# Optimization experiments

Hardware: AMD Instinct MI355X
Metric: run time of the kernel (lower is better)

The kernel has to match this reference:

```python
import jax, jax.numpy as jnp
import numpy as np

# Model hyperparams (match init_kwargs)
D_MODEL = 1024
D_STATE = 128
D_CONV = 4
EXPAND = 2
HEADDIM = 64
NGROUPS = 1
D_INNER = EXPAND * D_MODEL          # 2048
D_SSM = D_INNER                     # d_ssm=None -> d_inner; d_mlp = 0
NHEADS = D_SSM // HEADDIM           # 32
CONV_DIM = D_SSM + 2 * NGROUPS * D_STATE            # 2304
D_IN_PROJ = 2 * D_INNER + 2 * NGROUPS * D_STATE + NHEADS  # 4384
GROUP_SIZE = D_SSM // NGROUPS
EPS = 1e-5
HEAD_TO_GROUP = np.arange(NHEADS) // (NHEADS // NGROUPS)


def silu(x):
    return x * jax.nn.sigmoid(x)


def setup_inputs() -> dict:
    key = jax.random.key(0)
    ks = jax.random.split(key, 10)
    B, L = 16, 512
    u = jax.random.normal(ks[0], (B, L, D_MODEL), jnp.float32)
    # in_proj (bias=False): weight [d_in_proj, d_model]
    W_in = jax.random.normal(ks[1], (D_IN_PROJ, D_MODEL), jnp.float32) / np.sqrt(D_MODEL)
    # depthwise causal conv1d: weight [conv_dim, 1, d_conv], bias [conv_dim]
    conv_w = jax.random.normal(ks[2], (CONV_DIM, 1, D_CONV), jnp.float32) / np.sqrt(D_CONV)
    conv_b = jax.random.normal(ks[3], (CONV_DIM,), jnp.float32) * 0.01
    # recurrent feedback weights (zero-init in torch; small random here to exercise the path)
    W_rxbc = jax.random.normal(ks[4], (CONV_DIM, D_SSM), jnp.float32) * (0.01 / np.sqrt(D_SSM))
    W_rdt = jax.random.normal(ks[5], (NHEADS, D_SSM), jnp.float32) * (0.01 / np.sqrt(D_SSM))
    # dt_bias = inverse-softplus of dt ~ U_log[1e-3, 1e-1]
    dt = jnp.exp(jax.random.uniform(ks[6], (NHEADS,)) * (np.log(0.1) - np.log(0.001)) + np.log(0.001))
    dt_bias = dt + jnp.log(-jnp.expm1(-dt))
    A_log = jnp.log(jax.random.uniform(ks[7], (NHEADS,), minval=1.0, maxval=16.0))
    D_param = jnp.ones((NHEADS,), jnp.float32)
    norm_w = jnp.ones((D_SSM,), jnp.float32)
    W_out = jax.random.normal(ks[8], (D_MODEL, D_INNER), jnp.float32) / np.sqrt(D_INNER)
    return dict(u=u, W_in=W_in, conv_w=conv_w, conv_b=conv_b, W_rxbc=W_rxbc,
                W_rdt=W_rdt, dt_bias=dt_bias, A_log=A_log, D_param=D_param,
                norm_w=norm_w, W_out=W_out)


def _forward(u, W_in, conv_w, conv_b, W_rxbc, W_rdt, dt_bias, A_log, D_param, norm_w, W_out):
    B, L, _ = u.shape
    zxbcdt = jnp.einsum('bld,ed->ble', u, W_in)  # [B,L,d_in_proj]; d_mlp=0 so no z0/x0
    z, xBC_u, dt_raw = jnp.split(zxbcdt, [D_SSM, D_SSM + CONV_DIM], axis=-1)
    # causal depthwise conv over time (torch Conv1d pad=d_conv-1, truncated to L)
    xp = jnp.pad(xBC_u, ((0, 0), (D_CONV - 1, 0), (0, 0)))
    xBC_conv = conv_b + sum(xp[:, k:k + L, :] * conv_w[:, 0, k] for k in range(D_CONV))
    A = -jnp.exp(A_log.astype(jnp.float32))  # [H]

    def step(carry, inp):
        state, y_prev = carry            # state: [B,H,P,N] f32, y_prev: [B,d_ssm]
        xBC_t, dt_t, z_t = inp
        xBC = silu(xBC_t + y_prev @ W_rxbc.T)        # recurrent xBC feedback
        dtr = silu(dt_t + y_prev @ W_rdt.T)          # recurrent dt feedback
        x_t = xBC[:, :D_SSM]
        Bv = xBC[:, D_SSM:D_SSM + NGROUPS * D_STATE]
        Cv = xBC[:, D_SSM + NGROUPS * D_STATE:]
        dt = jax.nn.softplus(dtr + dt_bias).astype(jnp.float32)  # [B,H]; dt_limit=(0,inf) -> no clamp
        dA = jnp.exp(dt * A)                                     # [B,H]
        x_h = x_t.reshape(B, NHEADS, HEADDIM).astype(jnp.float32)
        B_hn = Bv.reshape(B, NGROUPS, D_STATE).astype(jnp.float32)[:, HEAD_TO_GROUP, :]
        C_hn = Cv.reshape(B, NGROUPS, D_STATE).astype(jnp.float32)[:, HEAD_TO_GROUP, :]
        state = state * dA[:, :, None, None] + dt[:, :, None, None] * x_h[:, :, :, None] * B_hn[:, :, None, :]
        y = (state * C_hn[:, :, None, :]).sum(-1) + D_param[None, :, None] * x_h  # [B,H,P]
        y = y.reshape(B, D_SSM)
        # gated RMSNorm (norm_before_gate=False): rmsnorm(y*silu(z)) * weight, groupwise
        g = y * silu(z_t)
        gg = g.reshape(B, NGROUPS, GROUP_SIZE)
        ms = jnp.mean(gg * gg, axis=-1, keepdims=True)
        yn = (gg * jax.lax.rsqrt(ms + EPS)).reshape(B, D_SSM) * norm_w
        out_t = yn @ W_out.T
        return (state, yn), out_t

    state0 = jnp.zeros((B, NHEADS, HEADDIM, D_STATE), jnp.float32)
    y0 = jnp.zeros((B, D_SSM), u.dtype)
    xs = (jnp.swapaxes(xBC_conv, 0, 1), jnp.swapaxes(dt_raw, 0, 1), jnp.swapaxes(z, 0, 1))
    _, out = jax.lax.scan(step, (state0, y0), xs)  # out: [L,B,d_model]
    return jnp.swapaxes(out, 0, 1)


def reference(u, W_in, conv_w, conv_b, W_rxbc, W_rdt, dt_bias, A_log, D_param, norm_w, W_out):
    return _forward(u, W_in, conv_w, conv_b, W_rxbc, W_rdt, dt_bias, A_log, D_param, norm_w, W_out)
```

## Files before the change

### kernel.cpp

```cpp
#include <hip/hip_runtime.h>

typedef __attribute__((ext_vector_type(8))) short short8;
typedef __attribute__((ext_vector_type(4))) float floatx4;

#define BQ 16
#define LQ 512
#define DM 1024
#define DPROJ 4384
#define RAWC 2336
#define KD 2048
#define NWG 128
#define NTHR 512
#define AWG 73

#define AFLAG_BASE 16384
#define BAR_U32 35072

__device__ __forceinline__ float siluf(float x) { return x / (1.f + __expf(-x)); }
__device__ __forceinline__ float softplusf(float x) { return (x > 20.f) ? x : log1pf(__expf(x)); }
__device__ __forceinline__ unsigned short f2bf(float f) {
    union { float f; unsigned u; } v; v.f = f;
    unsigned r = v.u + 0x7FFFu + ((v.u >> 16) & 1u);
    return (unsigned short)(r >> 16);
}

__global__ void cvt_bf16_kernel(const float* __restrict__ s, unsigned short* __restrict__ d, int n) {
    int i = blockIdx.x * 256 + threadIdx.x;
    if (i < n) d[i] = f2bf(s[i]);
}

__global__ void pack_weights_kernel(const float* __restrict__ rxbc, const float* __restrict__ rdt,
                                    const float* __restrict__ wout, unsigned short* __restrict__ wall) {
    long i = (long)blockIdx.x * 256 + threadIdx.x;
    if (i >= 3360L * KD) return;
    int c = (int)(i >> 11), k = (int)(i & 2047);
    const float* src = (c < 2304) ? rxbc + (long)c * KD + k
                     : (c < 2336) ? rdt + (long)(c - 2304) * KD + k
                     :              wout + (long)(c - 2336) * KD + k;
    wall[i] = f2bf(*src);
}

__global__ __launch_bounds__(256) void gemm_inproj_kernel(const short* __restrict__ A,
                                                          const short* __restrict__ Bw,
                                                          float* __restrict__ C) {
    const int lane = threadIdx.x & 63, wave = threadIdx.x >> 6;
    const int row = lane & 15, q = lane >> 4;
    const long m0 = (long)blockIdx.x * 128 + wave * 16;
    const long n0 = (long)blockIdx.y * 32;
    const short* ap0 = A + (m0 + row) * DM + q * 8;
    const short* ap1 = ap0 + 64 * DM;
    const short* bp0 = Bw + (n0 + row) * DM + q * 8;
    const short* bp1 = bp0 + 16 * DM;
    floatx4 acc00 = {0.f,0.f,0.f,0.f}, acc01 = {0.f,0.f,0.f,0.f};
    floatx4 acc10 = {0.f,0.f,0.f,0.f}, acc11 = {0.f,0.f,0.f,0.f};
    for (int k = 0; k < DM; k += 32) {
        short8 a0 = *(const short8*)(ap0 + k);
        short8 a1 = *(const short8*)(ap1 + k);
        short8 b0 = *(const short8*)(bp0 + k);
        short8 b1 = *(const short8*)(bp1 + k);
        acc00 = __builtin_amdgcn_mfma_f32_16x16x32_bf16(a0, b0, acc00, 0, 0, 0);
        acc01 = __builtin_amdgcn_mfma_f32_16x16x32_bf16(a0, b1, acc01, 0, 0, 0);
        acc10 = __builtin_amdgcn_mfma_f32_16x16x32_bf16(a1, b0, acc10, 0, 0, 0);
        acc11 = __builtin_amdgcn_mfma_f32_16x16x32_bf16(a1, b1, acc11, 0, 0, 0);
    }
    float* cp0 = C + (m0 + q * 4) * DPROJ + n0 + row;
    float* cp1 = cp0 + 64 * DPROJ;
    #pragma unroll
    for (int r = 0; r < 4; ++r) {
        cp0[(long)r * DPROJ]      = acc00[r];
        cp0[(long)r * DPROJ + 16] = acc01[r];
        cp1[(long)r * DPROJ]      = acc10[r];
        cp1[(long)r * DPROJ + 16] = acc11[r];
    }
}

__global__ void setup_zero_kernel(unsigned* ghist, float* msum, unsigned* bar) {
    int i = blockIdx.x * 256 + threadIdx.x;
    if (i < 16384) ghist[i] = 0u;
    if (i < 4096) msum[i] = 0.f;
    if (i < BAR_U32) bar[i] = 0u;
}

__global__ __launch_bounds__(NTHR, 1) void scan_kernel(
    const float* __restrict__ zx,
    float* __restrict__ raw,
    unsigned short* __restrict__ ghist,
    float* __restrict__ msum,
    unsigned* __restrict__ bar,
    const short* __restrict__ wall,
    float* __restrict__ scale_hist,
    const float* __restrict__ dt_bias, const float* __restrict__ A_log,
    const float* __restrict__ D_param, const float* __restrict__ norm_w,
    const float* __restrict__ conv_w, const float* __restrict__ conv_b,
    float* __restrict__ out)
{
    const int w = blockIdx.x, tid = threadIdx.x;
    const int lane = tid & 63, wv = tid >> 6;

    __shared__ float redu[2][8][16][16];
    __shared__ float bc_lds[2][128];
    __shared__ float ypart[4][64];

    const bool doA = (w < AWG);
    const int colr = lane & 15, q = lane >> 4;
    const unsigned long long* gq = (const unsigned long long*)ghist;
    const int abase = colr * 512 + wv * 64 + q * 2;
    const int r_tl = tid >> 8, r_idx = tid & 255, r_orow = r_idx >> 4, r_col = r_idx & 15;
    const unsigned* aspin = bar + ((((lane >> 2) * 8 + wv) * 4) + (lane & 3)) * 32;

    short8 wr0[8], wr1[8];
    if (doA) {
        const short* wp0 = wall + ((long)((2 * w    ) * 16 + colr) * KD + wv * 256 + q * 8);
        const short* wp1 = wall + ((long)((2 * w + 1) * 16 + colr) * KD + wv * 256 + q * 8);
        #pragma unroll
        for (int ks = 0; ks < 8; ++ks) {
            wr0[ks] = *(const short8*)(wp0 + ks * 32);
            wr1[ks] = *(const short8*)(wp1 + ks * 32);
        }
    }

    const int b = w >> 3;
    const int j = w & 7;
    const int h = j * 4 + (wv >> 1);
    const int half = wv & 1;
    float s[64];
    #pragma unroll
    for (int i = 0; i < 64; ++i) s[i] = 0.f;
    const float Aneg = -__expf(A_log[h]);
    const float dtb  = dt_bias[h];
    const float Dp   = D_param[h];
    const float nw   = norm_w[h * 64 + lane];
    const int cx = h * 64 + lane;
    const float4 cwx = *(const float4*)(conv_w + cx * 4);
    const float cbx = conv_b[cx];
    const int bcw = tid >> 7, bcn = tid & 127;
    const int cbc = 2048 + bcw * 128 + bcn;
    float4 cwbc = {0.f,0.f,0.f,0.f}; float cbbc = 0.f;
    if (tid < 256) { cwbc = *(const float4*)(conv_w + cbc * 4); cbbc = conv_b[cbc]; }
    float xh1 = 0.f, xh2 = 0.f, xh3 = 0.f, bh1 = 0.f, bh2 = 0.f, bh3 = 0.f;

    int sp_off = -1; unsigned sp_base = 0;
    {
        const int bq4 = b >> 2;
        if      (lane == 0) { sp_off = AFLAG_BASE + ((2*h  )*8 +     bq4) * 32; sp_base = 1; }
        else if (lane == 1) { sp_off = AFLAG_BASE + ((2*h+1)*8 +     bq4) * 32; sp_base = 1; }
        else if (lane == 2) { sp_off = AFLAG_BASE + ((2*h  )*8 + 4 + bq4) * 32; sp_base = 1; }
        else if (lane == 3) { sp_off = AFLAG_BASE + ((2*h+1)*8 + 4 + bq4) * 32; sp_base = 1; }
        else if (lane == 4) { sp_off = AFLAG_BASE + (72*8 + (h >= 16 ? 4 : 0) + bq4) * 32; sp_base = 1; }
        else if (wv < 4 && lane == 5) { sp_off = AFLAG_BASE + ((64+2*wv)*8 +     bq4) * 32; sp_base = 1; }
        else if (wv < 4 && lane == 6) { sp_off = AFLAG_BASE + ((65+2*wv)*8 +     bq4) * 32; sp_base = 1; }
        else if (wv < 4 && lane == 7) { sp_off = AFLAG_BASE + ((64+2*wv)*8 + 4 + bq4) * 32; sp_base = 1; }
        else if (wv < 4 && lane == 8) { sp_off = AFLAG_BASE + ((65+2*wv)*8 + 4 + bq4) * 32; sp_base = 1; }
        else if (lane >= 9 && lane < 41) {
            sp_off = ((b * 8 + ((lane - 9) >> 2)) * 4 + ((lane - 9) & 3)) * 32; sp_base = 0;
        }
    }
    const unsigned* bspin = bar + (sp_off < 0 ? 0 : sp_off);

    for (int t = 0; t < LQ; ++t) {
        const long zr = ((long)b * LQ + t) * DPROJ;
        float xq  = zx[zr + 2048 + cx];
        float zq  = zx[zr + cx];
        float dzq = zx[zr + 4352 + h];
        float bq = 0.f;
        if (tid < 256) bq = zx[zr + 2048 + cbc];

        if (doA) {
            while (__hip_atomic_load(aspin, __ATOMIC_RELAXED, __HIP_MEMORY_SCOPE_AGENT)
                   < (unsigned)t) {}
            unsigned long long ar[16];
            const long gb0 = (long)t * 8192 + abase;
            #pragma unroll
            for (int ks = 0; ks < 8; ++ks) {
                ar[2 * ks]     = __hip_atomic_load(gq + gb0 + ks * 8,
                                 __ATOMIC_RELAXED, __HIP_MEMORY_SCOPE_AGENT);
                ar[2 * ks + 1] = __hip_atomic_load(gq + gb0 + ks * 8 + 1,
                                 __ATOMIC_RELAXED, __HIP_MEMORY_SCOPE_AGENT);
            }
            floatx4 acc0 = {0.f,0.f,0.f,0.f}, acc1 = {0.f,0.f,0.f,0.f};
            #pragma unroll
            for (int ks = 0; ks < 8; ++ks) {
                union { unsigned long long u[2]; short8 s8; } af;
                af.u[0] = ar[2 * ks]; af.u[1] = ar[2 * ks + 1];
                acc0 = __builtin_amdgcn_mfma_f32_16x16x32_bf16(af.s8, wr0[ks], acc0, 0, 0, 0);
                acc1 = __builtin_amdgcn_mfma_f32_16x16x32_bf16(af.s8, wr1[ks], acc1, 0, 0, 0);
            }
            #pragma unroll
            for (int r = 0; r < 4; ++r) {
                redu[0][wv][q * 4 + r][colr] = acc0[r];
                redu[1][wv][q * 4 + r][colr] = acc1[r];
            }
            __syncthreads();
            float v = 0.f;
            #pragma unroll
            for (int kq = 0; kq < 8; ++kq) v += redu[r_tl][kq][r_orow][r_col];
            int gc = (2 * w + r_tl) * 16 + r_col;
            __hip_atomic_store(raw + (t & 1) * (16 * RAWC) + r_orow * RAWC + gc, v,
                               __ATOMIC_RELAXED, __HIP_MEMORY_SCOPE_AGENT);
            asm volatile("s_waitcnt vmcnt(0)" ::: "memory");
            if (lane == 0)
                __hip_atomic_store(bar + AFLAG_BASE + (w * 8 + wv) * 32, (unsigned)(t + 1),
                                   __ATOMIC_RELAXED, __HIP_MEMORY_SCOPE_AGENT);
            __syncthreads();
        }

        if (sp_off >= 0) {
            while (__hip_atomic_load(bspin, __ATOMIC_RELAXED, __HIP_MEMORY_SCOPE_AGENT)
                   < sp_base + (unsigned)t) {}
        }
        const float* rawb = raw + (t & 1) * (16 * RAWC) + b * RAWC;
        float bcval = 0.f;
        if (tid < 256) bcval = __hip_atomic_load(rawb + 2048 + bcw * 128 + bcn,
                                                 __ATOMIC_RELAXED, __HIP_MEMORY_SCOPE_AGENT);
        float xr   = __hip_atomic_load(rawb + cx,       __ATOMIC_RELAXED, __HIP_MEMORY_SCOPE_AGENT);
        float dtrr = __hip_atomic_load(rawb + 2304 + h, __ATOMIC_RELAXED, __HIP_MEMORY_SCOPE_AGENT);
        const float* mp = msum + ((t + 7) & 7) * 512 + b * 32;
        float msv = 0.f;
        #pragma unroll
        for (int k = 0; k < 32; ++k)
            msv += __hip_atomic_load(mp + k, __ATOMIC_RELAXED, __HIP_MEMORY_SCOPE_AGENT);
        float rs = rsqrtf(msv * (1.f / 2048.f) + 1e-5f);
        if (j == 0 && tid == 0 && t >= 1)
            __hip_atomic_store(scale_hist + b * LQ + (t - 1), rs,
                               __ATOMIC_RELAXED, __HIP_MEMORY_SCOPE_AGENT);
        if (tid < 256) {
            float pre = cbbc + bh3 * cwbc.x + bh2 * cwbc.y + bh1 * cwbc.z + bq * cwbc.w;
            bc_lds[bcw][bcn] = siluf(pre + rs * bcval);
            bh3 = bh2; bh2 = bh1; bh1 = bq;
        }
        float xpre = cbx + xh3 * cwx.x + xh2 * cwx.y + xh1 * cwx.z + xq * cwx.w;
        xh3 = xh2; xh2 = xh1; xh1 = xq;
        float xv = siluf(xpre + rs * xr);
        float dt = softplusf(siluf(dzq + rs * dtrr) + dtb);
        float dA = __expf(dt * Aneg);
        float zg = siluf(zq);
        __syncthreads();

        float dtx = dt * xv, yac = 0.f;
        const floatx4* Bp = (const floatx4*)&bc_lds[0][half * 64];
        const floatx4* Cp = (const floatx4*)&bc_lds[1][half * 64];
        #pragma unroll
        for (int i = 0; i < 16; ++i) {
            floatx4 b4 = Bp[i], c4 = Cp[i];
            s[4*i+0] = s[4*i+0] * dA + dtx * b4.x; yac += s[4*i+0] * c4.x;
            s[4*i+1] = s[4*i+1] * dA + dtx * b4.y; yac += s[4*i+1] * c4.y;
            s[4*i+2] = s[4*i+2] * dA + dtx * b4.z; yac += s[4*i+2] * c4.z;
            s[4*i+3] = s[4*i+3] * dA + dtx * b4.w; yac += s[4*i+3] * c4.w;
        }
        if (half) ypart[wv >> 1][lane] = yac;
        __syncthreads();
        if (!half) {
            float y = yac + ypart[wv >> 1][lane] + Dp * xv;
            float g = y * zg;
            unsigned gb = (unsigned)f2bf(g * nw);
            unsigned up = __shfl_down(gb, 1);
            if (!(lane & 1))
                __hip_atomic_store((unsigned*)ghist + ((long)(t + 1) * 16384
                                   + ((b * KD + h * 64 + lane) >> 1)),
                                   gb | (up << 16), __ATOMIC_RELAXED, __HIP_MEMORY_SCOPE_AGENT);
            float sq = g * g;
            #pragma unroll
            for (int off = 32; off; off >>= 1) sq += __shfl_xor(sq, off, 64);
            if (lane == 0)
                __hip_atomic_store(msum + ((t & 7) * 512 + b * 32 + j * 4 + (wv >> 1)), sq,
                                   __ATOMIC_RELAXED, __HIP_MEMORY_SCOPE_AGENT);
            asm volatile("s_waitcnt vmcnt(0)" ::: "memory");
            if (lane == 0)
                __hip_atomic_store(bar + (w * 4 + (wv >> 1)) * 32, (unsigned)(t + 1),
                                   __ATOMIC_RELAXED, __HIP_MEMORY_SCOPE_AGENT);
        }
    }

    {
        const unsigned* fp = bar + tid * 32;
        while (__hip_atomic_load(fp, __ATOMIC_RELAXED, __HIP_MEMORY_SCOPE_AGENT) < 512u) {}
    }
    __syncthreads();
    {
        const int vb = w * 2 + (tid >> 8);
        const int vt = tid & 255;
        const int vwv = vt >> 6, vlane = vt & 63;
        const int vcolr = vlane & 15, vq = vlane >> 4;
        for (int it = 0; it < 8; ++it) {
            const int idx = vb * 8 + it;
            const int tt = idx >> 2;
            const int n0 = (idx & 3) * 256 + vwv * 64;
            const long ab = (long)(tt + 1) * 8192 + vcolr * 512 + vq * 2;
            const short* bp = wall + ((long)(2336 + n0 + vcolr) * KD + vq * 8);
            const unsigned long long* gq2 = (const unsigned long long*)ghist;
            floatx4 acc0 = {0.f,0.f,0.f,0.f}, acc1 = {0.f,0.f,0.f,0.f};
            floatx4 acc2 = {0.f,0.f,0.f,0.f}, acc3 = {0.f,0.f,0.f,0.f};
            #pragma unroll 4
            for (int kb = 0; kb < 64; ++kb) {
                unsigned long long a0 = __hip_atomic_load(gq2 + ab + kb * 8,
                                        __ATOMIC_RELAXED, __HIP_MEMORY_SCOPE_AGENT);
                unsigned long long a1 = __hip_atomic_load(gq2 + ab + kb * 8 + 1,
                                        __ATOMIC_RELAXED, __HIP_MEMORY_SCOPE_AGENT);
                union { unsigned long long u[2]; short8 s8; } af;
                af.u[0] = a0; af.u[1] = a1;
                const short* bk = bp + kb * 32;
                acc0 = __builtin_amdgcn_mfma_f32_16x16x32_bf16(af.s8, *(const short8*)(bk),           acc0, 0, 0, 0);
                acc1 = __builtin_amdgcn_mfma_f32_16x16x32_bf16(af.s8, *(const short8*)(bk + 16 * KD), acc1, 0, 0, 0);
                acc2 = __builtin_amdgcn_mfma_f32_16x16x32_bf16(af.s8, *(const short8*)(bk + 32 * KD), acc2, 0, 0, 0);
                acc3 = __builtin_amdgcn_mfma_f32_16x16x32_bf16(af.s8, *(const short8*)(bk + 48 * KD), acc3, 0, 0, 0);
            }
            #pragma unroll
            for (int r = 0; r < 4; ++r) {
                const int bb = vq * 4 + r;
                float sc;
                if (tt < LQ - 1) {
                    sc = __hip_atomic_load(scale_hist + bb * LQ + tt,
                                           __ATOMIC_RELAXED, __HIP_MEMORY_SCOPE_AGENT);
                } else {
                    float msv = 0.f;
                    #pragma unroll
                    for (int k = 0; k < 32; ++k)
                        msv += __hip_atomic_load(msum + 7 * 512 + bb * 32 + k,
                                                 __ATOMIC_RELAXED, __HIP_MEMORY_SCOPE_AGENT);
                    sc = rsqrtf(msv * (1.f / 2048.f) + 1e-5f);
                }
                float* op = out + ((long)bb * LQ + tt) * DM + n0 + vcolr;
                op[0]  = acc0[r] * sc;
                op[16] = acc1[r] * sc;
                op[32] = acc2[r] * sc;
                op[48] = acc3[r] * sc;
            }
        }
    }
}

extern "C" void kernel_launch(void* const* d_in, const int* in_sizes, int n_in,
                              void* d_out, int out_size, void* d_ws, size_t ws_size,
                              hipStream_t stream) {
    const float* u       = (const float*)d_in[0];
    const float* W_in    = (const float*)d_in[1];
    const float* conv_w  = (const float*)d_in[2];
    const float* conv_b  = (const float*)d_in[3];
    const float* W_rxbc  = (const float*)d_in[4];
    const float* W_rdt   = (const float*)d_in[5];
    const float* dt_bias = (const float*)d_in[6];
    const float* A_log   = (const float*)d_in[7];
    const float* D_param = (const float*)d_in[8];
    const float* norm_w  = (const float*)d_in[9];
    const float* W_out   = (const float*)d_in[10];
    float* out = (float*)d_out;

    char* ws = (char*)d_ws;
    size_t off = 0;
    auto alloc = [&](size_t bytes) -> void* {
        void* p = ws + off; off += (bytes + 255) & ~(size_t)255; return p;
    };
    float* zx            = (float*)alloc((size_t)BQ * LQ * DPROJ * 4);
    unsigned short* u_bf = (unsigned short*)alloc((size_t)BQ * LQ * DM * 2);
    unsigned short* w_bf = (unsigned short*)alloc((size_t)DPROJ * DM * 2);
    unsigned short* gh   = (unsigned short*)alloc((size_t)(LQ + 1) * BQ * KD * 2);
    float* msum          = (float*)alloc(4096 * 4);
    float* raw           = (float*)alloc(2 * (size_t)BQ * RAWC * 4);
    float* scale_hist    = (float*)alloc((size_t)BQ * LQ * 4);
    unsigned* bar        = (unsigned*)alloc((size_t)BAR_U32 * 4);

    { int n = BQ * LQ * DM; cvt_bf16_kernel<<<(n + 255) / 256, 256, 0, stream>>>(u, u_bf, n); }
    { int n = DPROJ * DM;   cvt_bf16_kernel<<<(n + 255) / 256, 256, 0, stream>>>(W_in, w_bf, n); }
    gemm_inproj_kernel<<<dim3(BQ * LQ / 128, DPROJ / 32), 256, 0, stream>>>(
        (const short*)u_bf, (const short*)w_bf, zx);
    unsigned short* wall = u_bf;
    { long n = 3360L * KD;
      pack_weights_kernel<<<(int)((n + 255) / 256), 256, 0, stream>>>(W_rxbc, W_rdt, W_out, wall); }
    setup_zero_kernel<<<(BAR_U32 + 255) / 256, 256, 0, stream>>>((unsigned*)gh, msum, bar);

    void* args[] = { &zx, &raw, &gh, &msum, &bar, &wall, &scale_hist,
                     &dt_bias, &A_log, &D_param, &norm_w, &conv_w, &conv_b, &out };
    hipLaunchCooperativeKernel((void*)scan_kernel, dim3(NWG), dim3(NTHR), args, 0, stream);
}
```

Baseline: 6.303 ms.

## Replace flag barriers with epoch-tagged 64-bit values in persistent scan

The per-step cross-workgroup handoffs in the persistent scan kernel no longer use separate counter flags followed by data reads. Each value (gated output history, raw recurrent projections, mean-square partials) is now written as a 64-bit word carrying the payload and a timestep tag, so consumers spin directly on the data until the tags match. The LDS reduction across waves in the recurrent GEMM is removed; each wave writes its own partial, and consumers sum 8 partials themselves. This removes flag round-trips, vmcnt waits and two __syncthreads per step, at the cost of doubled storage and traffic for the tagged buffers and more polling loads.

New measurement: 13.72 ms. 2.18x slower.

```diff
diff --git a/kernel.cpp b/kernel.cpp
--- a/kernel.cpp
+++ b/kernel.cpp
@@ -13,8 +13,10 @@
 #define NTHR 512
 #define AWG 73
 
-#define AFLAG_BASE 16384
-#define BAR_U32 35072
+#define RAWP_WSTRIDE 37376
+#define RAWP_SLOT   299008
+#define TAG_SLOT     16384
+#define MSUM_SLOT      512
 
 __device__ __forceinline__ float siluf(float x) { return x / (1.f + __expf(-x)); }
 __device__ __forceinline__ float softplusf(float x) { return (x > 20.f) ? x : log1pf(__expf(x)); }
@@ -23,6 +25,23 @@
     unsigned r = v.u + 0x7FFFu + ((v.u >> 16) & 1u);
     return (unsigned short)(r >> 16);
 }
+__device__ __forceinline__ unsigned long long ld64(const unsigned long long* p) {
+    return __hip_atomic_load(p, __ATOMIC_RELAXED, __HIP_MEMORY_SCOPE_AGENT);
+}
+__device__ __forceinline__ void st64(unsigned long long* p, unsigned long long v) {
+    __hip_atomic_store(p, v, __ATOMIC_RELAXED, __HIP_MEMORY_SCOPE_AGENT);
+}
+__device__ __forceinline__ unsigned long long packf(float f, unsigned e) {
+    union { float f; unsigned u; } v; v.f = f;
+    return ((unsigned long long)e << 32) | v.u;
+}
+__device__ __forceinline__ unsigned long long packu(unsigned payload, unsigned e) {
+    return ((unsigned long long)e << 32) | payload;
+}
+__device__ __forceinline__ float lof(unsigned long long w) {
+    union { unsigned u; float f; } v; v.u = (unsigned)w; return v.f;
+}
+__device__ __forceinline__ unsigned hie(unsigned long long w) { return (unsigned)(w >> 32); }
 
 __global__ void cvt_bf16_kernel(const float* __restrict__ s, unsigned short* __restrict__ d, int n) {
     int i = blockIdx.x * 256 + threadIdx.x;
@@ -38,6 +57,11 @@
                      : (c < 2336) ? rdt + (long)(c - 2304) * KD + k
                      :              wout + (long)(c - 2336) * KD + k;
     wall[i] = f2bf(*src);
+}
+
+__global__ void setup_zero_kernel(unsigned* __restrict__ base, long n) {
+    long i = (long)blockIdx.x * 256 + threadIdx.x;
+    for (; i < n; i += (long)gridDim.x * 256) base[i] = 0u;
 }
 
 __global__ __launch_bounds__(256) void gemm_inproj_kernel(const short* __restrict__ A,
@@ -74,18 +98,12 @@
     }
 }
 
-__global__ void setup_zero_kernel(unsigned* ghist, float* msum, unsigned* bar) {
-    int i = blockIdx.x * 256 + threadIdx.x;
-    if (i < 16384) ghist[i] = 0u;
-    if (i < 4096) msum[i] = 0.f;
-    if (i < BAR_U32) bar[i] = 0u;
-}
-
 __global__ __launch_bounds__(NTHR, 1) void scan_kernel(
     const float* __restrict__ zx,
-    float* __restrict__ raw,
+    unsigned long long* __restrict__ rawP,
     unsigned short* __restrict__ ghist,
-    float* __restrict__ msum,
+    unsigned long long* __restrict__ tagged,
+    unsigned long long* __restrict__ msum,
     unsigned* __restrict__ bar,
     const short* __restrict__ wall,
     float* __restrict__ scale_hist,
@@ -97,16 +115,11 @@
     const int w = blockIdx.x, tid = threadIdx.x;
     const int lane = tid & 63, wv = tid >> 6;
 
-    __shared__ float redu[2][8][16][16];
     __shared__ float bc_lds[2][128];
     __shared__ float ypart[4][64];
 
     const bool doA = (w < AWG);
     const int colr = lane & 15, q = lane >> 4;
-    const unsigned long long* gq = (const unsigned long long*)ghist;
-    const int abase = colr * 512 + wv * 64 + q * 2;
-    const int r_tl = tid >> 8, r_idx = tid & 255, r_orow = r_idx >> 4, r_col = r_idx & 15;
-    const unsigned* aspin = bar + ((((lane >> 2) * 8 + wv) * 4) + (lane & 3)) * 32;
 
     short8 wr0[8], wr1[8];
     if (doA) {
@@ -139,25 +152,8 @@
     if (tid < 256) { cwbc = *(const float4*)(conv_w + cbc * 4); cbbc = conv_b[cbc]; }
     float xh1 = 0.f, xh2 = 0.f, xh3 = 0.f, bh1 = 0.f, bh2 = 0.f, bh3 = 0.f;
 
-    int sp_off = -1; unsigned sp_base = 0;
-    {
-        const int bq4 = b >> 2;
-        if      (lane == 0) { sp_off = AFLAG_BASE + ((2*h  )*8 +     bq4) * 32; sp_base = 1; }
-        else if (lane == 1) { sp_off = AFLAG_BASE + ((2*h+1)*8 +     bq4) * 32; sp_base = 1; }
-        else if (lane == 2) { sp_off = AFLAG_BASE + ((2*h  )*8 + 4 + bq4) * 32; sp_base = 1; }
-        else if (lane == 3) { sp_off = AFLAG_BASE + ((2*h+1)*8 + 4 + bq4) * 32; sp_base = 1; }
-        else if (lane == 4) { sp_off = AFLAG_BASE + (72*8 + (h >= 16 ? 4 : 0) + bq4) * 32; sp_base = 1; }
-        else if (wv < 4 && lane == 5) { sp_off = AFLAG_BASE + ((64+2*wv)*8 +     bq4) * 32; sp_base = 1; }
-        else if (wv < 4 && lane == 6) { sp_off = AFLAG_BASE + ((65+2*wv)*8 +     bq4) * 32; sp_base = 1; }
-        else if (wv < 4 && lane == 7) { sp_off = AFLAG_BASE + ((64+2*wv)*8 + 4 + bq4) * 32; sp_base = 1; }
-        else if (wv < 4 && lane == 8) { sp_off = AFLAG_BASE + ((65+2*wv)*8 + 4 + bq4) * 32; sp_base = 1; }
-        else if (lane >= 9 && lane < 41) {
-            sp_off = ((b * 8 + ((lane - 9) >> 2)) * 4 + ((lane - 9) & 3)) * 32; sp_base = 0;
-        }
-    }
-    const unsigned* bspin = bar + (sp_off < 0 ? 0 : sp_off);
-
     for (int t = 0; t < LQ; ++t) {
+        const unsigned eR = (unsigned)(t + 1);
         const long zr = ((long)b * LQ + t) * DPROJ;
         float xq  = zx[zr + 2048 + cx];
         float zq  = zx[zr + cx];
@@ -166,64 +162,113 @@
         if (tid < 256) bq = zx[zr + 2048 + cbc];
 
         if (doA) {
-            while (__hip_atomic_load(aspin, __ATOMIC_RELAXED, __HIP_MEMORY_SCOPE_AGENT)
-                   < (unsigned)t) {}
-            unsigned long long ar[16];
-            const long gb0 = (long)t * 8192 + abase;
+            const unsigned et = (unsigned)t;
+            const unsigned long long* tg = tagged + (long)(t & 1) * TAG_SLOT
+                                           + colr * 1024 + wv * 128 + q * 4;
+            while (true) {
+                unsigned bad = 0;
+                #pragma unroll
+                for (int ks = 0; ks < 8; ++ks)
+                    bad |= hie(ld64(tg + ks * 16 + 3)) ^ et;
+                if (!__any(bad != 0u)) break;
+            }
+            unsigned long long aw[32];
             #pragma unroll
             for (int ks = 0; ks < 8; ++ks) {
-                ar[2 * ks]     = __hip_atomic_load(gq + gb0 + ks * 8,
-                                 __ATOMIC_RELAXED, __HIP_MEMORY_SCOPE_AGENT);
-                ar[2 * ks + 1] = __hip_atomic_load(gq + gb0 + ks * 8 + 1,
-                                 __ATOMIC_RELAXED, __HIP_MEMORY_SCOPE_AGENT);
+                #pragma unroll
+                for (int c = 0; c < 4; ++c)
+                    aw[ks * 4 + c] = ld64(tg + ks * 16 + c);
+            }
+            while (true) {
+                unsigned bad = 0;
+                #pragma unroll
+                for (int i = 0; i < 32; ++i) bad |= hie(aw[i]) ^ et;
+                if (!__any(bad != 0u)) break;
+                #pragma unroll
+                for (int ks = 0; ks < 8; ++ks) {
+                    #pragma unroll
+                    for (int c = 0; c < 4; ++c)
+                        if (hie(aw[ks * 4 + c]) != et)
+                            aw[ks * 4 + c] = ld64(tg + ks * 16 + c);
+                }
             }
             floatx4 acc0 = {0.f,0.f,0.f,0.f}, acc1 = {0.f,0.f,0.f,0.f};
             #pragma unroll
             for (int ks = 0; ks < 8; ++ks) {
-                union { unsigned long long u[2]; short8 s8; } af;
-                af.u[0] = ar[2 * ks]; af.u[1] = ar[2 * ks + 1];
+                union { unsigned u[4]; short8 s8; } af;
+                af.u[0] = (unsigned)aw[ks*4+0]; af.u[1] = (unsigned)aw[ks*4+1];
+                af.u[2] = (unsigned)aw[ks*4+2]; af.u[3] = (unsigned)aw[ks*4+3];
                 acc0 = __builtin_amdgcn_mfma_f32_16x16x32_bf16(af.s8, wr0[ks], acc0, 0, 0, 0);
                 acc1 = __builtin_amdgcn_mfma_f32_16x16x32_bf16(af.s8, wr1[ks], acc1, 0, 0, 0);
             }
+            unsigned long long* rp = rawP + (long)(t & 1) * RAWP_SLOT + wv * RAWP_WSTRIDE;
+            const int c0 = 32 * w + colr;
             #pragma unroll
             for (int r = 0; r < 4; ++r) {
-                redu[0][wv][q * 4 + r][colr] = acc0[r];
-                redu[1][wv][q * 4 + r][colr] = acc1[r];
-            }
-            __syncthreads();
-            float v = 0.f;
-            #pragma unroll
-            for (int kq = 0; kq < 8; ++kq) v += redu[r_tl][kq][r_orow][r_col];
-            int gc = (2 * w + r_tl) * 16 + r_col;
-            __hip_atomic_store(raw + (t & 1) * (16 * RAWC) + r_orow * RAWC + gc, v,
-                               __ATOMIC_RELAXED, __HIP_MEMORY_SCOPE_AGENT);
-            asm volatile("s_waitcnt vmcnt(0)" ::: "memory");
-            if (lane == 0)
-                __hip_atomic_store(bar + AFLAG_BASE + (w * 8 + wv) * 32, (unsigned)(t + 1),
-                                   __ATOMIC_RELAXED, __HIP_MEMORY_SCOPE_AGENT);
-            __syncthreads();
-        }
-
-        if (sp_off >= 0) {
-            while (__hip_atomic_load(bspin, __ATOMIC_RELAXED, __HIP_MEMORY_SCOPE_AGENT)
-                   < sp_base + (unsigned)t) {}
-        }
-        const float* rawb = raw + (t & 1) * (16 * RAWC) + b * RAWC;
-        float bcval = 0.f;
-        if (tid < 256) bcval = __hip_atomic_load(rawb + 2048 + bcw * 128 + bcn,
-                                                 __ATOMIC_RELAXED, __HIP_MEMORY_SCOPE_AGENT);
-        float xr   = __hip_atomic_load(rawb + cx,       __ATOMIC_RELAXED, __HIP_MEMORY_SCOPE_AGENT);
-        float dtrr = __hip_atomic_load(rawb + 2304 + h, __ATOMIC_RELAXED, __HIP_MEMORY_SCOPE_AGENT);
-        const float* mp = msum + ((t + 7) & 7) * 512 + b * 32;
-        float msv = 0.f;
+                const int bb = q * 4 + r;
+                st64(rp + bb * 2336 + c0,      packf(acc0[r], eR));
+                st64(rp + bb * 2336 + c0 + 16, packf(acc1[r], eR));
+            }
+        }
+
+        const unsigned long long* rbase = rawP + (long)(t & 1) * RAWP_SLOT + (long)b * 2336;
+        unsigned long long xw[8];
         #pragma unroll
-        for (int k = 0; k < 32; ++k)
-            msv += __hip_atomic_load(mp + k, __ATOMIC_RELAXED, __HIP_MEMORY_SCOPE_AGENT);
-        float rs = rsqrtf(msv * (1.f / 2048.f) + 1e-5f);
+        for (int p = 0; p < 8; ++p) xw[p] = ld64(rbase + p * RAWP_WSTRIDE + cx);
+        unsigned long long bw_[8];
+        if (tid < 256) {
+            #pragma unroll
+            for (int p = 0; p < 8; ++p) bw_[p] = ld64(rbase + p * RAWP_WSTRIDE + cbc);
+        }
+        float mv = 0.f, dvp = 0.f;
+        if (lane < 32) {
+            const unsigned long long* mp = msum + ((t + 1) & 1) * MSUM_SLOT + b * 32 + lane;
+            unsigned long long wd = ld64(mp);
+            while (hie(wd) != (unsigned)t) wd = ld64(mp);
+            mv = lof(wd);
+        } else if (lane < 40) {
+            const unsigned long long* dp = rbase + (lane - 32) * RAWP_WSTRIDE + 2304 + h;
+            unsigned long long wd = ld64(dp);
+            while (hie(wd) != eR) wd = ld64(dp);
+            dvp = lof(wd);
+        }
+        float msv = mv;
+        #pragma unroll
+        for (int off = 32; off; off >>= 1) msv += __shfl_xor(msv, off, 64);
+        float dsum = dvp;
+        dsum += __shfl_xor(dsum, 1, 64);
+        dsum += __shfl_xor(dsum, 2, 64);
+        dsum += __shfl_xor(dsum, 4, 64);
+        const float dtrr = __shfl(dsum, 32, 64);
+        const float rs = rsqrtf(msv * (1.f / 2048.f) + 1e-5f);
         if (j == 0 && tid == 0 && t >= 1)
             __hip_atomic_store(scale_hist + b * LQ + (t - 1), rs,
                                __ATOMIC_RELAXED, __HIP_MEMORY_SCOPE_AGENT);
+        while (true) {
+            unsigned bad = 0;
+            #pragma unroll
+            for (int p = 0; p < 8; ++p) bad |= hie(xw[p]) ^ eR;
+            if (!__any(bad != 0u)) break;
+            #pragma unroll
+            for (int p = 0; p < 8; ++p)
+                if (hie(xw[p]) != eR) xw[p] = ld64(rbase + p * RAWP_WSTRIDE + cx);
+        }
+        float xr = 0.f;
+        #pragma unroll
+        for (int p = 0; p < 8; ++p) xr += lof(xw[p]);
         if (tid < 256) {
+            while (true) {
+                unsigned bad = 0;
+                #pragma unroll
+                for (int p = 0; p < 8; ++p) bad |= hie(bw_[p]) ^ eR;
+                if (!__any(bad != 0u)) break;
+                #pragma unroll
+                for (int p = 0; p < 8; ++p)
+                    if (hie(bw_[p]) != eR) bw_[p] = ld64(rbase + p * RAWP_WSTRIDE + cbc);
+            }
+            float bcval = 0.f;
+            #pragma unroll
+            for (int p = 0; p < 8; ++p) bcval += lof(bw_[p]);
             float pre = cbbc + bh3 * cwbc.x + bh2 * cwbc.y + bh1 * cwbc.z + bq * cwbc.w;
             bc_lds[bcw][bcn] = siluf(pre + rs * bcval);
             bh3 = bh2; bh2 = bh1; bh1 = bq;
@@ -254,26 +299,28 @@
             float g = y * zg;
             unsigned gb = (unsigned)f2bf(g * nw);
             unsigned up = __shfl_down(gb, 1);
-            if (!(lane & 1))
-                __hip_atomic_store((unsigned*)ghist + ((long)(t + 1) * 16384
-                                   + ((b * KD + h * 64 + lane) >> 1)),
-                                   gb | (up << 16), __ATOMIC_RELAXED, __HIP_MEMORY_SCOPE_AGENT);
+            if (!(lane & 1)) {
+                const long pidx = ((long)b * 1024 + ((h * 64 + lane) >> 1));
+                unsigned packed = gb | (up << 16);
+                __hip_atomic_store((unsigned*)ghist + ((long)(t + 1) * 16384 + pidx), packed,
+                                   __ATOMIC_RELAXED, __HIP_MEMORY_SCOPE_AGENT);
+                st64(tagged + ((long)((t + 1) & 1) * TAG_SLOT + pidx), packu(packed, eR));
+            }
             float sq = g * g;
             #pragma unroll
             for (int off = 32; off; off >>= 1) sq += __shfl_xor(sq, off, 64);
             if (lane == 0)
-                __hip_atomic_store(msum + ((t & 7) * 512 + b * 32 + j * 4 + (wv >> 1)), sq,
-                                   __ATOMIC_RELAXED, __HIP_MEMORY_SCOPE_AGENT);
-            asm volatile("s_waitcnt vmcnt(0)" ::: "memory");
-            if (lane == 0)
-                __hip_atomic_store(bar + (w * 4 + (wv >> 1)) * 32, (unsigned)(t + 1),
-                                   __ATOMIC_RELAXED, __HIP_MEMORY_SCOPE_AGENT);
-        }
-    }
-
-    {
+                st64(msum + ((t & 1) * MSUM_SLOT + b * 32 + j * 4 + (wv >> 1)), packf(sq, eR));
+        }
+    }
+
+    asm volatile("s_waitcnt vmcnt(0)" ::: "memory");
+    __syncthreads();
+    if (tid == 0)
+        __hip_atomic_store(bar + w * 32, 1u, __ATOMIC_RELAXED, __HIP_MEMORY_SCOPE_AGENT);
+    if (tid < 128) {
         const unsigned* fp = bar + tid * 32;
-        while (__hip_atomic_load(fp, __ATOMIC_RELAXED, __HIP_MEMORY_SCOPE_AGENT) < 512u) {}
+        while (__hip_atomic_load(fp, __ATOMIC_RELAXED, __HIP_MEMORY_SCOPE_AGENT) < 1u) {}
     }
     __syncthreads();
     {
@@ -281,21 +328,19 @@
         const int vt = tid & 255;
         const int vwv = vt >> 6, vlane = vt & 63;
         const int vcolr = vlane & 15, vq = vlane >> 4;
+        const unsigned long long* gq2 = (const unsigned long long*)ghist;
         for (int it = 0; it < 8; ++it) {
             const int idx = vb * 8 + it;
             const int tt = idx >> 2;
             const int n0 = (idx & 3) * 256 + vwv * 64;
             const long ab = (long)(tt + 1) * 8192 + vcolr * 512 + vq * 2;
             const short* bp = wall + ((long)(2336 + n0 + vcolr) * KD + vq * 8);
-            const unsigned long long* gq2 = (const unsigned long long*)ghist;
             floatx4 acc0 = {0.f,0.f,0.f,0.f}, acc1 = {0.f,0.f,0.f,0.f};
             floatx4 acc2 = {0.f,0.f,0.f,0.f}, acc3 = {0.f,0.f,0.f,0.f};
             #pragma unroll 4
             for (int kb = 0; kb < 64; ++kb) {
-                unsigned long long a0 = __hip_atomic_load(gq2 + ab + kb * 8,
-                                        __ATOMIC_RELAXED, __HIP_MEMORY_SCOPE_AGENT);
-                unsigned long long a1 = __hip_atomic_load(gq2 + ab + kb * 8 + 1,
-                                        __ATOMIC_RELAXED, __HIP_MEMORY_SCOPE_AGENT);
+                unsigned long long a0 = ld64(gq2 + ab + kb * 8);
+                unsigned long long a1 = ld64(gq2 + ab + kb * 8 + 1);
                 union { unsigned long long u[2]; short8 s8; } af;
                 af.u[0] = a0; af.u[1] = a1;
                 const short* bk = bp + kb * 32;
@@ -315,8 +360,7 @@
                     float msv = 0.f;
                     #pragma unroll
                     for (int k = 0; k < 32; ++k)
-                        msv += __hip_atomic_load(msum + 7 * 512 + bb * 32 + k,
-                                                 __ATOMIC_RELAXED, __HIP_MEMORY_SCOPE_AGENT);
+                        msv += lof(ld64(msum + 1 * MSUM_SLOT + bb * 32 + k));
                     sc = rsqrtf(msv * (1.f / 2048.f) + 1e-5f);
                 }
                 float* op = out + ((long)bb * LQ + tt) * DM + n0 + vcolr;
@@ -354,10 +398,15 @@
     unsigned short* u_bf = (unsigned short*)alloc((size_t)BQ * LQ * DM * 2);
     unsigned short* w_bf = (unsigned short*)alloc((size_t)DPROJ * DM * 2);
     unsigned short* gh   = (unsigned short*)alloc((size_t)(LQ + 1) * BQ * KD * 2);
-    float* msum          = (float*)alloc(4096 * 4);
-    float* raw           = (float*)alloc(2 * (size_t)BQ * RAWC * 4);
+    unsigned long long* tagged = (unsigned long long*)alloc((size_t)2 * TAG_SLOT * 8);
+    unsigned long long* msum   = (unsigned long long*)alloc((size_t)2 * MSUM_SLOT * 8);
+    unsigned long long* rawP   = (unsigned long long*)alloc((size_t)2 * RAWP_SLOT * 8);
+    unsigned* bar        = (unsigned*)alloc(128 * 32 * 4);
     float* scale_hist    = (float*)alloc((size_t)BQ * LQ * 4);
-    unsigned* bar        = (unsigned*)alloc((size_t)BAR_U32 * 4);
+
+    const long zero_u32 = ((size_t)2 * TAG_SLOT * 8 + (size_t)2 * MSUM_SLOT * 8
+                           + (size_t)2 * RAWP_SLOT * 8 + 128 * 32 * 4) / 4;
+    setup_zero_kernel<<<2048, 256, 0, stream>>>((unsigned*)tagged, zero_u32);
 
     { int n = BQ * LQ * DM; cvt_bf16_kernel<<<(n + 255) / 256, 256, 0, stream>>>(u, u_bf, n); }
     { int n = DPROJ * DM;   cvt_bf16_kernel<<<(n + 255) / 256, 256, 0, stream>>>(W_in, w_bf, n); }
@@ -366,9 +415,8 @@
     unsigned short* wall = u_bf;
     { long n = 3360L * KD;
       pack_weights_kernel<<<(int)((n + 255) / 256), 256, 0, stream>>>(W_rxbc, W_rdt, W_out, wall); }
-    setup_zero_kernel<<<(BAR_U32 + 255) / 256, 256, 0, stream>>>((unsigned*)gh, msum, bar);
-
-    void* args[] = { &zx, &raw, &gh, &msum, &bar, &wall, &scale_hist,
+
+    void* args[] = { &zx, &rawP, &gh, &tagged, &msum, &bar, &wall, &scale_hist,
                      &dt_bias, &A_log, &D_param, &norm_w, &conv_w, &conv_b, &out };
     hipLaunchCooperativeKernel((void*)scan_kernel, dim3(NWG), dim3(NTHR), args, 0, stream);
 }
```

## Replace flag-based spin barriers with epoch-tagged 64-bit value words

Applied to the files above, without the earlier changes.

Cross-workgroup data (the recurrent projection outputs and the RMS partial sums) is now written as 64-bit words that pack the float value with a step epoch. Consumers spin directly on the data word until the epoch matches, so the separate flag stores, the vmcnt waits and the block-wide syncthreads on the producer side go away. The msum reduction is now spread across 32 lanes with a shuffle instead of one thread doing 32 serial loads. In exchange the buffers double in size and every consumer lane polls memory on its own, which adds L2 traffic and polling contention.

New measurement: 5.754 ms. -8.7%, faster.

```diff
diff --git a/kernel.cpp b/kernel.cpp
--- a/kernel.cpp
+++ b/kernel.cpp
@@ -13,8 +13,8 @@
 #define NTHR 512
 #define AWG 73
 
-#define AFLAG_BASE 16384
-#define BAR_U32 35072
+#define RAWT_SLOT 37376
+#define MSUM_SLOT 512
 
 __device__ __forceinline__ float siluf(float x) { return x / (1.f + __expf(-x)); }
 __device__ __forceinline__ float softplusf(float x) { return (x > 20.f) ? x : log1pf(__expf(x)); }
@@ -23,6 +23,20 @@
     unsigned r = v.u + 0x7FFFu + ((v.u >> 16) & 1u);
     return (unsigned short)(r >> 16);
 }
+__device__ __forceinline__ unsigned long long ld64(const unsigned long long* p) {
+    return __hip_atomic_load(p, __ATOMIC_RELAXED, __HIP_MEMORY_SCOPE_AGENT);
+}
+__device__ __forceinline__ void st64(unsigned long long* p, unsigned long long v) {
+    __hip_atomic_store(p, v, __ATOMIC_RELAXED, __HIP_MEMORY_SCOPE_AGENT);
+}
+__device__ __forceinline__ unsigned long long packf(float f, unsigned e) {
+    union { float f; unsigned u; } v; v.f = f;
+    return ((unsigned long long)e << 32) | v.u;
+}
+__device__ __forceinline__ float lof(unsigned long long w) {
+    union { unsigned u; float f; } v; v.u = (unsigned)w; return v.f;
+}
+__device__ __forceinline__ unsigned hie(unsigned long long w) { return (unsigned)(w >> 32); }
 
 __global__ void cvt_bf16_kernel(const float* __restrict__ s, unsigned short* __restrict__ d, int n) {
     int i = blockIdx.x * 256 + threadIdx.x;
@@ -38,6 +52,13 @@
                      : (c < 2336) ? rdt + (long)(c - 2304) * KD + k
                      :              wout + (long)(c - 2336) * KD + k;
     wall[i] = f2bf(*src);
+}
+
+__global__ void setup_zero_kernel(unsigned* __restrict__ z, long nz, unsigned* __restrict__ gh0) {
+    long i = (long)blockIdx.x * 256 + threadIdx.x;
+    const long stride = (long)gridDim.x * 256;
+    for (long k = i; k < nz; k += stride) z[k] = 0u;
+    if (i < 16384) gh0[i] = 0u;
 }
 
 __global__ __launch_bounds__(256) void gemm_inproj_kernel(const short* __restrict__ A,
@@ -74,18 +95,11 @@
     }
 }
 
-__global__ void setup_zero_kernel(unsigned* ghist, float* msum, unsigned* bar) {
-    int i = blockIdx.x * 256 + threadIdx.x;
-    if (i < 16384) ghist[i] = 0u;
-    if (i < 4096) msum[i] = 0.f;
-    if (i < BAR_U32) bar[i] = 0u;
-}
-
 __global__ __launch_bounds__(NTHR, 1) void scan_kernel(
     const float* __restrict__ zx,
-    float* __restrict__ raw,
+    unsigned long long* __restrict__ rawT,
     unsigned short* __restrict__ ghist,
-    float* __restrict__ msum,
+    unsigned long long* __restrict__ msum,
     unsigned* __restrict__ bar,
     const short* __restrict__ wall,
     float* __restrict__ scale_hist,
@@ -139,25 +153,8 @@
     if (tid < 256) { cwbc = *(const float4*)(conv_w + cbc * 4); cbbc = conv_b[cbc]; }
     float xh1 = 0.f, xh2 = 0.f, xh3 = 0.f, bh1 = 0.f, bh2 = 0.f, bh3 = 0.f;
 
-    int sp_off = -1; unsigned sp_base = 0;
-    {
-        const int bq4 = b >> 2;
-        if      (lane == 0) { sp_off = AFLAG_BASE + ((2*h  )*8 +     bq4) * 32; sp_base = 1; }
-        else if (lane == 1) { sp_off = AFLAG_BASE + ((2*h+1)*8 +     bq4) * 32; sp_base = 1; }
-        else if (lane == 2) { sp_off = AFLAG_BASE + ((2*h  )*8 + 4 + bq4) * 32; sp_base = 1; }
-        else if (lane == 3) { sp_off = AFLAG_BASE + ((2*h+1)*8 + 4 + bq4) * 32; sp_base = 1; }
-        else if (lane == 4) { sp_off = AFLAG_BASE + (72*8 + (h >= 16 ? 4 : 0) + bq4) * 32; sp_base = 1; }
-        else if (wv < 4 && lane == 5) { sp_off = AFLAG_BASE + ((64+2*wv)*8 +     bq4) * 32; sp_base = 1; }
-        else if (wv < 4 && lane == 6) { sp_off = AFLAG_BASE + ((65+2*wv)*8 +     bq4) * 32; sp_base = 1; }
-        else if (wv < 4 && lane == 7) { sp_off = AFLAG_BASE + ((64+2*wv)*8 + 4 + bq4) * 32; sp_base = 1; }
-        else if (wv < 4 && lane == 8) { sp_off = AFLAG_BASE + ((65+2*wv)*8 + 4 + bq4) * 32; sp_base = 1; }
-        else if (lane >= 9 && lane < 41) {
-            sp_off = ((b * 8 + ((lane - 9) >> 2)) * 4 + ((lane - 9) & 3)) * 32; sp_base = 0;
-        }
-    }
-    const unsigned* bspin = bar + (sp_off < 0 ? 0 : sp_off);
-
     for (int t = 0; t < LQ; ++t) {
+        const unsigned eR = (unsigned)(t + 1);
         const long zr = ((long)b * LQ + t) * DPROJ;
         float xq  = zx[zr + 2048 + cx];
         float zq  = zx[zr + cx];
@@ -172,10 +169,8 @@
             const long gb0 = (long)t * 8192 + abase;
             #pragma unroll
             for (int ks = 0; ks < 8; ++ks) {
-                ar[2 * ks]     = __hip_atomic_load(gq + gb0 + ks * 8,
-                                 __ATOMIC_RELAXED, __HIP_MEMORY_SCOPE_AGENT);
-                ar[2 * ks + 1] = __hip_atomic_load(gq + gb0 + ks * 8 + 1,
-                                 __ATOMIC_RELAXED, __HIP_MEMORY_SCOPE_AGENT);
+                ar[2 * ks]     = ld64(gq + gb0 + ks * 8);
+                ar[2 * ks + 1] = ld64(gq + gb0 + ks * 8 + 1);
             }
             floatx4 acc0 = {0.f,0.f,0.f,0.f}, acc1 = {0.f,0.f,0.f,0.f};
             #pragma unroll
@@ -194,36 +189,36 @@
             float v = 0.f;
             #pragma unroll
             for (int kq = 0; kq < 8; ++kq) v += redu[r_tl][kq][r_orow][r_col];
-            int gc = (2 * w + r_tl) * 16 + r_col;
-            __hip_atomic_store(raw + (t & 1) * (16 * RAWC) + r_orow * RAWC + gc, v,
-                               __ATOMIC_RELAXED, __HIP_MEMORY_SCOPE_AGENT);
-            asm volatile("s_waitcnt vmcnt(0)" ::: "memory");
-            if (lane == 0)
-                __hip_atomic_store(bar + AFLAG_BASE + (w * 8 + wv) * 32, (unsigned)(t + 1),
-                                   __ATOMIC_RELAXED, __HIP_MEMORY_SCOPE_AGENT);
-            __syncthreads();
-        }
-
-        if (sp_off >= 0) {
-            while (__hip_atomic_load(bspin, __ATOMIC_RELAXED, __HIP_MEMORY_SCOPE_AGENT)
-                   < sp_base + (unsigned)t) {}
-        }
-        const float* rawb = raw + (t & 1) * (16 * RAWC) + b * RAWC;
-        float bcval = 0.f;
-        if (tid < 256) bcval = __hip_atomic_load(rawb + 2048 + bcw * 128 + bcn,
-                                                 __ATOMIC_RELAXED, __HIP_MEMORY_SCOPE_AGENT);
-        float xr   = __hip_atomic_load(rawb + cx,       __ATOMIC_RELAXED, __HIP_MEMORY_SCOPE_AGENT);
-        float dtrr = __hip_atomic_load(rawb + 2304 + h, __ATOMIC_RELAXED, __HIP_MEMORY_SCOPE_AGENT);
-        const float* mp = msum + ((t + 7) & 7) * 512 + b * 32;
-        float msv = 0.f;
+            const int gc = (2 * w + r_tl) * 16 + r_col;
+            st64(rawT + (long)(t & 1) * RAWT_SLOT + r_orow * 2336 + gc, packf(v, eR));
+        }
+
+        const unsigned long long* rbase = rawT + (long)(t & 1) * RAWT_SLOT + (long)b * 2336;
+        unsigned long long xw = ld64(rbase + cx);
+        unsigned long long dw = ld64(rbase + 2304 + h);
+        unsigned long long bw = 0;
+        if (tid < 256) bw = ld64(rbase + cbc);
+        float mv = 0.f;
+        if (lane < 32) {
+            const unsigned long long* mp = msum + ((t + 7) & 7) * MSUM_SLOT + b * 32 + lane;
+            unsigned long long wd = ld64(mp);
+            while (hie(wd) != (unsigned)t) wd = ld64(mp);
+            mv = lof(wd);
+        }
+        float msv = mv;
         #pragma unroll
-        for (int k = 0; k < 32; ++k)
-            msv += __hip_atomic_load(mp + k, __ATOMIC_RELAXED, __HIP_MEMORY_SCOPE_AGENT);
-        float rs = rsqrtf(msv * (1.f / 2048.f) + 1e-5f);
+        for (int off = 32; off; off >>= 1) msv += __shfl_xor(msv, off, 64);
+        const float rs = rsqrtf(msv * (1.f / 2048.f) + 1e-5f);
         if (j == 0 && tid == 0 && t >= 1)
             __hip_atomic_store(scale_hist + b * LQ + (t - 1), rs,
                                __ATOMIC_RELAXED, __HIP_MEMORY_SCOPE_AGENT);
+        while (hie(xw) != eR) xw = ld64(rbase + cx);
+        const float xr = lof(xw);
+        while (hie(dw) != eR) dw = ld64(rbase + 2304 + h);
+        const float dtrr = lof(dw);
         if (tid < 256) {
+            while (hie(bw) != eR) bw = ld64(rbase + cbc);
+            float bcval = lof(bw);
             float pre = cbbc + bh3 * cwbc.x + bh2 * cwbc.y + bh1 * cwbc.z + bq * cwbc.w;
             bc_lds[bcw][bcn] = siluf(pre + rs * bcval);
             bh3 = bh2; bh2 = bh1; bh1 = bq;
@@ -262,8 +257,7 @@
             #pragma unroll
             for (int off = 32; off; off >>= 1) sq += __shfl_xor(sq, off, 64);
             if (lane == 0)
-                __hip_atomic_store(msum + ((t & 7) * 512 + b * 32 + j * 4 + (wv >> 1)), sq,
-                                   __ATOMIC_RELAXED, __HIP_MEMORY_SCOPE_AGENT);
+                st64(msum + ((t & 7) * MSUM_SLOT + b * 32 + j * 4 + (wv >> 1)), packf(sq, eR));
             asm volatile("s_waitcnt vmcnt(0)" ::: "memory");
             if (lane == 0)
                 __hip_atomic_store(bar + (w * 4 + (wv >> 1)) * 32, (unsigned)(t + 1),
@@ -281,21 +275,19 @@
         const int vt = tid & 255;
         const int vwv = vt >> 6, vlane = vt & 63;
         const int vcolr = vlane & 15, vq = vlane >> 4;
+        const unsigned long long* gq2 = (const unsigned long long*)ghist;
         for (int it = 0; it < 8; ++it) {
             const int idx = vb * 8 + it;
             const int tt = idx >> 2;
             const int n0 = (idx & 3) * 256 + vwv * 64;
             const long ab = (long)(tt + 1) * 8192 + vcolr * 512 + vq * 2;
             const short* bp = wall + ((long)(2336 + n0 + vcolr) * KD + vq * 8);
-            const unsigned long long* gq2 = (const unsigned long long*)ghist;
             floatx4 acc0 = {0.f,0.f,0.f,0.f}, acc1 = {0.f,0.f,0.f,0.f};
             floatx4 acc2 = {0.f,0.f,0.f,0.f}, acc3 = {0.f,0.f,0.f,0.f};
             #pragma unroll 4
             for (int kb = 0; kb < 64; ++kb) {
-                unsigned long long a0 = __hip_atomic_load(gq2 + ab + kb * 8,
-                                        __ATOMIC_RELAXED, __HIP_MEMORY_SCOPE_AGENT);
-                unsigned long long a1 = __hip_atomic_load(gq2 + ab + kb * 8 + 1,
-                                        __ATOMIC_RELAXED, __HIP_MEMORY_SCOPE_AGENT);
+                unsigned long long a0 = ld64(gq2 + ab + kb * 8);
+                unsigned long long a1 = ld64(gq2 + ab + kb * 8 + 1);
                 union { unsigned long long u[2]; short8 s8; } af;
                 af.u[0] = a0; af.u[1] = a1;
                 const short* bk = bp + kb * 32;
@@ -315,8 +307,7 @@
                     float msv = 0.f;
                     #pragma unroll
                     for (int k = 0; k < 32; ++k)
-                        msv += __hip_atomic_load(msum + 7 * 512 + bb * 32 + k,
-                                                 __ATOMIC_RELAXED, __HIP_MEMORY_SCOPE_AGENT);
+                        msv += lof(ld64(msum + 7 * MSUM_SLOT + bb * 32 + k));
                     sc = rsqrtf(msv * (1.f / 2048.f) + 1e-5f);
                 }
                 float* op = out + ((long)bb * LQ + tt) * DM + n0 + vcolr;
@@ -354,10 +345,14 @@
     unsigned short* u_bf = (unsigned short*)alloc((size_t)BQ * LQ * DM * 2);
     unsigned short* w_bf = (unsigned short*)alloc((size_t)DPROJ * DM * 2);
     unsigned short* gh   = (unsigned short*)alloc((size_t)(LQ + 1) * BQ * KD * 2);
-    float* msum          = (float*)alloc(4096 * 4);
-    float* raw           = (float*)alloc(2 * (size_t)BQ * RAWC * 4);
+    unsigned long long* rawT = (unsigned long long*)alloc((size_t)2 * RAWT_SLOT * 8);
+    unsigned long long* msum = (unsigned long long*)alloc((size_t)8 * MSUM_SLOT * 8);
+    unsigned* bar        = (unsigned*)alloc(16384 * 4);
     float* scale_hist    = (float*)alloc((size_t)BQ * LQ * 4);
-    unsigned* bar        = (unsigned*)alloc((size_t)BAR_U32 * 4);
+
+    const long zero_u32 = ((size_t)2 * RAWT_SLOT * 8 + (size_t)8 * MSUM_SLOT * 8
+                           + (size_t)16384 * 4) / 4;
+    setup_zero_kernel<<<680, 256, 0, stream>>>((unsigned*)rawT, zero_u32, (unsigned*)gh);
 
     { int n = BQ * LQ * DM; cvt_bf16_kernel<<<(n + 255) / 256, 256, 0, stream>>>(u, u_bf, n); }
     { int n = DPROJ * DM;   cvt_bf16_kernel<<<(n + 255) / 256, 256, 0, stream>>>(W_in, w_bf, n); }
@@ -366,9 +361,8 @@
     unsigned short* wall = u_bf;
     { long n = 3360L * KD;
       pack_weights_kernel<<<(int)((n + 255) / 256), 256, 0, stream>>>(W_rxbc, W_rdt, W_out, wall); }
-    setup_zero_kernel<<<(BAR_U32 + 255) / 256, 256, 0, stream>>>((unsigned*)gh, msum, bar);
-
-    void* args[] = { &zx, &raw, &gh, &msum, &bar, &wall, &scale_hist,
+
+    void* args[] = { &zx, &rawT, &gh, &msum, &bar, &wall, &scale_hist,
                      &dt_bias, &A_log, &D_param, &norm_w, &conv_w, &conv_b, &out };
     hipLaunchCooperativeKernel((void*)scan_kernel, dim3(NWG), dim3(NTHR), args, 0, stream);
 }
```
